# Optimization experiments

Hardware: AMD Instinct MI355X
Metric: run time of the kernel (lower is better)

Reference implementation:

```python
import jax, jax.numpy as jnp
import numpy as np

B = 131072      # batch
IN = 1024       # input_dim
H = 384         # hidden[0]
L = 128         # latent_dim = hidden[1]
K = 32          # slots_k
R = 2           # top_r
TAU = 0.7


def setup_inputs() -> dict:
    key = jax.random.key(0)
    ks = jax.random.split(key, 8)
    s = 0.02
    f32 = jnp.float32
    return {
        "x":  jax.random.normal(ks[0], (B, IN), f32),
        "w1": jax.random.normal(ks[1], (IN, H), f32) * s,
        "b1": jnp.zeros((H,), f32),
        "w2": jax.random.normal(ks[2], (H, L), f32) * s,
        "b2": jnp.zeros((L,), f32),
        "mk": jax.random.normal(ks[3], (K, L), f32) * s,  # memory_keys
        "mv": jax.random.normal(ks[4], (K, L), f32) * s,  # memory_values
        "w3": jax.random.normal(ks[5], (2 * L, H), f32) * s,
        "b3": jnp.zeros((H,), f32),
        "w4": jax.random.normal(ks[6], (H, 1), f32) * s,
        "b4": jnp.zeros((1,), f32),
    }


def reference(x, w1, b1, w2, b2, mk, mv, w3, b3, w4, b4):
    # block_a: Linear -> GELU -> (Dropout=id in eval) -> Linear -> GELU
    z = jax.nn.gelu(x @ w1 + b1, approximate=False)
    z = jax.nn.gelu(z @ w2 + b2, approximate=False)          # [B, L]

    # top-r slot attention over memory bank
    logits = (z @ mk.T) / TAU                                 # [B, K]
    _, idx = jax.lax.top_k(logits, R)                         # [B, R]
    keep = jax.nn.one_hot(idx, K, dtype=logits.dtype).sum(-2) > 0  # [B, K] bool
    masked = jnp.where(keep, logits, -jnp.inf)
    attn = jax.nn.softmax(masked, axis=-1)                    # [B, K]
    mem = attn @ mv                                           # [B, L]

    fused = jnp.concatenate([z, mem], axis=-1)                # [B, 2L]

    # default head: Linear -> GELU -> Linear(.,1)
    h = jax.nn.gelu(fused @ w3 + b3, approximate=False)
    logit = (h @ w4 + b4)[..., 0]                             # [B]
    return jax.nn.sigmoid(logit)
```

## Files before the change

kernel.cpp:

```cpp
#include <hip/hip_runtime.h>

#define BATCH   131072
#define INDIM   1024
#define BM      64
#define BDIM    512
#define NBLK    (BATCH / BM)

#define WT_OFF   0
#define XT0_OFF  49152
#define XT1_OFF  57344
#define Z1_OFF   0
#define W2T0_OFF 50176
#define W2T1_OFF 58368
#define FZ_OFF   0
#define RP_OFF   33792
#define W3T_OFF  42240
#define CB_OFF   66816
#define B1S_OFF  (CB_OFF)
#define B2S_OFF  (CB_OFF + 1536)
#define B3S_OFF  (CB_OFF + 2048)
#define W4S_OFF  (CB_OFF + 3584)
#define MKS_OFF  (CB_OFF + 5120)
#define SMEM_BYTES (CB_OFF + 13824)

typedef unsigned short u16;
typedef u16    u16x8  __attribute__((ext_vector_type(8)));
typedef u16    u16x4  __attribute__((ext_vector_type(4)));
typedef __bf16 bf16x8 __attribute__((ext_vector_type(8)));
typedef __bf16 bf16x4 __attribute__((ext_vector_type(4)));
typedef float  f32x4  __attribute__((ext_vector_type(4)));

__device__ __forceinline__ u16 f2bf(float f) {
  unsigned u = __float_as_uint(f);
  u += 0x7FFFu + ((u >> 16) & 1u);
  return (u16)(u >> 16);
}

__device__ __forceinline__ float gelu_fast(float v) {
  float t = v * v;
  float u = v * fmaf(t, 0.0356774081f, 0.7978845608f);
  float e = __builtin_amdgcn_exp2f(u * -2.885390082f);
  return v * __builtin_amdgcn_rcpf(1.0f + e);
}

__device__ __forceinline__ f32x4 mfma16(u16x8 a, u16x8 b, f32x4 c) {
  return __builtin_amdgcn_mfma_f32_16x16x32_bf16(
      __builtin_bit_cast(bf16x8, a), __builtin_bit_cast(bf16x8, b), c, 0, 0, 0);
}

__device__ __forceinline__ u16x8 cvt8(float4 a, float4 b) {
  bf16x8 r;
  r[0]=(__bf16)a.x; r[1]=(__bf16)a.y; r[2]=(__bf16)a.z; r[3]=(__bf16)a.w;
  r[4]=(__bf16)b.x; r[5]=(__bf16)b.y; r[6]=(__bf16)b.z; r[7]=(__bf16)b.w;
  return __builtin_bit_cast(u16x8, r);
}
__device__ __forceinline__ u16x4 cvt4(float4 a) {
  bf16x4 r;
  r[0]=(__bf16)a.x; r[1]=(__bf16)a.y; r[2]=(__bf16)a.z; r[3]=(__bf16)a.w;
  return __builtin_bit_cast(u16x4, r);
}

typedef __attribute__((address_space(3))) unsigned int       lds_u32;
typedef __attribute__((address_space(1))) const unsigned int glb_u32;
__device__ __forceinline__ void gload16(const void* g, void* l) {
  __builtin_amdgcn_global_load_lds((glb_u32*)g, (lds_u32*)l, 16, 0, 0);
}

#define FENCE_SCHED __builtin_amdgcn_sched_barrier(0)
#define WAIT_LGKM0 do { asm volatile("s_waitcnt lgkmcnt(0)" ::: "memory"); FENCE_SCHED; } while (0)
#define WAIT_VMN(N) do { asm volatile("s_waitcnt vmcnt(" #N ")" ::: "memory"); FENCE_SCHED; } while (0)
#define BARRIER_LGKM do { \
  asm volatile("s_waitcnt lgkmcnt(0)" ::: "memory"); \
  __builtin_amdgcn_s_barrier(); FENCE_SCHED; } while (0)

__global__ void prep_kernel(const float* __restrict__ w1, const float* __restrict__ w2,
                            const float* __restrict__ w3, u16* __restrict__ w1s,
                            u16* __restrict__ w2s, u16* __restrict__ w3s) {
  int i = blockIdx.x * 256 + threadIdx.x;
  if (i < 393216) {
    int t = i / 24576, p = i % 24576;
    int r = p >> 6, q = p & 63, cp = q >> 3, o = q & 7;
    int k = t * 64 + ((cp ^ (r & 7)) << 3) + o;
    w1s[i] = f2bf(w1[k * 384 + r]);
  } else if (i < 442368) {
    int j = i - 393216;
    int t = j / 4096, p = j % 4096;
    int r = p >> 5, q = p & 31, cp = q >> 3, o = q & 7;
    int k = t * 32 + ((cp ^ ((r >> 1) & 3)) << 3) + o;
    w2s[j] = f2bf(w2[k * 128 + r]);
  } else if (i < 540672) {
    int j = i - 442368;
    int t = j / 12288, p = j % 12288;
    int r = p >> 5, q = p & 31, cp = q >> 3, o = q & 7;
    int k = t * 32 + ((cp ^ ((r >> 1) & 3)) << 3) + o;
    w3s[j] = f2bf(w3[k * 384 + r]);
  }
}

__global__ __launch_bounds__(BDIM, 4) void fused_kernel(
    const float* __restrict__ x,  const u16* __restrict__ w1s,
    const float* __restrict__ b1, const u16* __restrict__ w2s,
    const float* __restrict__ b2, const float* __restrict__ mkw,
    const float* __restrict__ mvw, const u16* __restrict__ w3s,
    const float* __restrict__ b3, const float* __restrict__ w4,
    const float* __restrict__ b4, float* __restrict__ out) {
  extern __shared__ char smem[];
  u16*   z1  = (u16*)(smem + Z1_OFF);
  u16*   fz  = (u16*)(smem + FZ_OFF);
  u16*   w3t = (u16*)(smem + W3T_OFF);
  float* b1s = (float*)(smem + B1S_OFF);
  float* b2s = (float*)(smem + B2S_OFF);
  float* b3s = (float*)(smem + B3S_OFF);
  float* w4s = (float*)(smem + W4S_OFF);
  u16*   mks = (u16*)(smem + MKS_OFF);
  float* rowpart = (float*)(smem + RP_OFF);

  const int tid  = threadIdx.x;
  const int lane = tid & 63;
  const int wid  = tid >> 6;
  const int l15  = lane & 15;
  const int g    = lane >> 4;
  const int swz8 = l15 & 7;
  const int swz4 = (l15 >> 1) & 3;
  const int row0 = blockIdx.x * BM;
  const int wrow = wid * 48;
  const int wstrip = wid * 3072;

  {
    const u16* ws = w1s + wstrip + lane * 8;
    u16* wd = (u16*)(smem + WT_OFF) + wstrip;
    #pragma unroll
    for (int i = 0; i < 6; ++i) gload16(ws + i * 512, wd + i * 512);
  }
  FENCE_SCHED;
  const int xrow = tid >> 3, xoct = tid & 7;
  const float* xp = x + (long)(row0 + xrow) * INDIM + xoct * 8;
  const int xdst = xrow * 64 + ((xoct ^ (xrow & 7)) << 3);
  float4 xa = *(const float4*)xp, xb = *(const float4*)(xp + 4);

  if (tid < 384) b1s[tid] = b1[tid];
  if (tid < 128) b2s[tid] = b2[tid];
  if (tid < 384) b3s[tid] = b3[tid];
  if (tid < 384) w4s[tid] = w4[tid];
  {
    int r = tid >> 4, cc = (tid & 15) * 8;
    const float4* p = (const float4*)(mkw + r * 128 + cc);
    *(u16x8*)(mks + r * 136 + cc) = cvt8(p[0], p[1]);
  }
  *(u16x8*)((u16*)(smem + XT0_OFF) + xdst) = cvt8(xa, xb);
  { const float* p = xp + 64; xa = *(const float4*)p; xb = *(const float4*)(p + 4); }
  BARRIER_LGKM;

  f32x4 acc[4][3];
  #pragma unroll
  for (int m = 0; m < 4; ++m)
    #pragma unroll
    for (int n = 0; n < 3; ++n) acc[m][n] = (f32x4){0.f, 0.f, 0.f, 0.f};

  const u16* wtb = (const u16*)(smem + WT_OFF);
  for (int kt = 0; kt < 16; ++kt) {
    if (kt < 15) { WAIT_VMN(2); } else { WAIT_VMN(0); }
    const u16* xtb = (const u16*)(smem + ((kt & 1) ? XT1_OFF : XT0_OFF));
    u16x8 af[4], bfr[3];
    const int c0 = (g ^ swz8) * 8;
    #pragma unroll
    for (int m = 0; m < 4; ++m) af[m] = *(const u16x8*)(xtb + (m * 16 + l15) * 64 + c0);
    #pragma unroll
    for (int n = 0; n < 3; ++n) bfr[n] = *(const u16x8*)(wtb + (wrow + n * 16 + l15) * 64 + c0);
    #pragma unroll
    for (int m = 0; m < 4; ++m)
      #pragma unroll
      for (int n = 0; n < 3; ++n) acc[m][n] = mfma16(bfr[n], af[m], acc[m][n]);
    const int c1 = ((g + 4) ^ swz8) * 8;
    #pragma unroll
    for (int m = 0; m < 4; ++m) af[m] = *(const u16x8*)(xtb + (m * 16 + l15) * 64 + c1);
    #pragma unroll
    for (int n = 0; n < 3; ++n) bfr[n] = *(const u16x8*)(wtb + (wrow + n * 16 + l15) * 64 + c1);
    WAIT_LGKM0;
    if (kt < 15) {
      const u16* ws = w1s + (kt + 1) * 24576 + wstrip + lane * 8;
      u16* wd = (u16*)(smem + WT_OFF) + wstrip;
      #pragma unroll
      for (int i = 0; i < 6; ++i) gload16(ws + i * 512, wd + i * 512);
      FENCE_SCHED;
      u16* xn = (u16*)(smem + ((kt & 1) ? XT0_OFF : XT1_OFF));
      *(u16x8*)(xn + xdst) = cvt8(xa, xb);
      if (kt < 14) {
        const float* p = xp + (kt + 2) * 64;
        xa = *(const float4*)p; xb = *(const float4*)(p + 4);
      }
      BARRIER_LGKM;
    }
    #pragma unroll
    for (int m = 0; m < 4; ++m)
      #pragma unroll
      for (int n = 0; n < 3; ++n) acc[m][n] = mfma16(bfr[n], af[m], acc[m][n]);
  }
  BARRIER_LGKM;

  {
    const u16* s2 = w2s + wid * 512 + lane * 8;
    gload16(s2, (u16*)(smem + W2T0_OFF) + wid * 512);
    const u16* s2b = w2s + 4096 + wid * 512 + lane * 8;
    gload16(s2b, (u16*)(smem + W2T1_OFF) + wid * 512);
  }
  #pragma unroll
  for (int m = 0; m < 4; ++m) {
    #pragma unroll
    for (int n = 0; n < 3; ++n) {
      int col = wrow + n * 16 + g * 4;
      float4 bv = *(const float4*)(b1s + col);
      f32x4 a = acc[m][n];
      float4 gv = {gelu_fast(a[0] + bv.x), gelu_fast(a[1] + bv.y),
                   gelu_fast(a[2] + bv.z), gelu_fast(a[3] + bv.w)};
      *(u16x4*)(z1 + (m * 16 + l15) * 392 + col) = cvt4(gv);
    }
  }
  BARRIER_LGKM;

  f32x4 acc2[4];
  #pragma unroll
  for (int m = 0; m < 4; ++m) acc2[m] = (f32x4){0.f, 0.f, 0.f, 0.f};
  for (int kt = 0; kt < 12; ++kt) {
    if (kt < 10) { WAIT_VMN(1); } else { WAIT_VMN(0); }
    const u16* wb = (const u16*)(smem + ((kt & 1) ? W2T1_OFF : W2T0_OFF));
    u16x8 a2f[4];
    #pragma unroll
    for (int m = 0; m < 4; ++m)
      a2f[m] = *(const u16x8*)(z1 + (m * 16 + l15) * 392 + kt * 32 + g * 8);
    u16x8 b2f = *(const u16x8*)(wb + (wid * 16 + l15) * 32 + (g ^ swz4) * 8);
    WAIT_LGKM0;
    if (kt < 10) {
      const u16* s2 = w2s + (kt + 2) * 4096 + wid * 512 + lane * 8;
      gload16(s2, (u16*)(smem + ((kt & 1) ? W2T1_OFF : W2T0_OFF)) + wid * 512);
    }
    #pragma unroll
    for (int m = 0; m < 4; ++m) acc2[m] = mfma16(b2f, a2f[m], acc2[m]);
  }
  BARRIER_LGKM;

  {
    const u16* s3 = w3s + wid * 1536 + lane * 8;
    u16* d3 = w3t + wid * 1536;
    gload16(s3, d3); gload16(s3 + 512, d3 + 512); gload16(s3 + 1024, d3 + 1024);
  }
  #pragma unroll
  for (int m = 0; m < 4; ++m) {
    int col = wid * 16 + g * 4;
    float4 bv = *(const float4*)(b2s + col);
    f32x4 a = acc2[m];
    float4 gv = {gelu_fast(a[0] + bv.x), gelu_fast(a[1] + bv.y),
                 gelu_fast(a[2] + bv.z), gelu_fast(a[3] + bv.w)};
    *(u16x4*)(fz + (m * 16 + l15) * 264 + col) = cvt4(gv);
  }
  BARRIER_LGKM;

  if (wid < 4) {
    const int wr = wid * 16 + l15;
    f32x4 accl[2] = {(f32x4){0,0,0,0}, (f32x4){0,0,0,0}};
    #pragma unroll
    for (int ks = 0; ks < 4; ++ks) {
      u16x8 afz = *(const u16x8*)(fz + wr * 264 + ks * 32 + g * 8);
      u16x8 k0  = *(const u16x8*)(mks + l15 * 136 + ks * 32 + g * 8);
      u16x8 k1  = *(const u16x8*)(mks + (16 + l15) * 136 + ks * 32 + g * 8);
      accl[0] = mfma16(k0, afz, accl[0]);
      accl[1] = mfma16(k1, afz, accl[1]);
    }
    float m1 = -3.4e38f, m2 = -3.4e38f; int i1 = -1, i2 = -1;
    #pragma unroll
    for (int n = 0; n < 2; ++n)
      #pragma unroll
      for (int j = 0; j < 4; ++j) {
        float v = accl[n][j]; int idx = n * 16 + g * 4 + j;
        if (v > m1) { m2 = m1; i2 = i1; m1 = v; i1 = idx; }
        else if (v > m2) { m2 = v; i2 = idx; }
      }
    #pragma unroll
    for (int d = 16; d <= 32; d <<= 1) {
      float om1 = __shfl_xor(m1, d); int oi1 = __shfl_xor(i1, d);
      float om2 = __shfl_xor(m2, d); int oi2 = __shfl_xor(i2, d);
      bool take = (om1 > m1) || (om1 == m1 && oi1 < i1);
      if (take) {
        float nm2; int ni2;
        if (m1 > om2 || (m1 == om2 && i1 < oi2)) { nm2 = m1; ni2 = i1; }
        else { nm2 = om2; ni2 = oi2; }
        m1 = om1; i1 = oi1; m2 = nm2; i2 = ni2;
      } else {
        if (om1 > m2 || (om1 == m2 && oi1 < i2)) { m2 = om1; i2 = oi1; }
      }
    }
    float a1 = __builtin_amdgcn_rcpf(
        1.0f + __builtin_amdgcn_exp2f((m2 - m1) * (1.44269504f / 0.7f)));
    float a2 = 1.0f - a1;
    const float* v1 = mvw + i1 * 128 + g * 32;
    const float* v2 = mvw + i2 * 128 + g * 32;
    #pragma unroll
    for (int c = 0; c < 4; ++c) {
      float4 A0 = *(const float4*)(v1 + c * 8), A1 = *(const float4*)(v1 + c * 8 + 4);
      float4 B0 = *(const float4*)(v2 + c * 8), B1 = *(const float4*)(v2 + c * 8 + 4);
      float4 r0 = {a1*A0.x + a2*B0.x, a1*A0.y + a2*B0.y, a1*A0.z + a2*B0.z, a1*A0.w + a2*B0.w};
      float4 r1 = {a1*A1.x + a2*B1.x, a1*A1.y + a2*B1.y, a1*A1.z + a2*B1.z, a1*A1.w + a2*B1.w};
      *(u16x8*)(fz + wr * 264 + 128 + g * 32 + c * 8) = cvt8(r0, r1);
    }
  }
  BARRIER_LGKM;

  f32x4 acc3[4][3];
  #pragma unroll
  for (int m = 0; m < 4; ++m)
    #pragma unroll
    for (int n = 0; n < 3; ++n) acc3[m][n] = (f32x4){0.f, 0.f, 0.f, 0.f};
  for (int kt = 0; kt < 8; ++kt) {
    WAIT_VMN(0);
    u16x8 a3f[4], b3f[3];
    #pragma unroll
    for (int m = 0; m < 4; ++m)
      a3f[m] = *(const u16x8*)(fz + (m * 16 + l15) * 264 + kt * 32 + g * 8);
    #pragma unroll
    for (int n = 0; n < 3; ++n)
      b3f[n] = *(const u16x8*)(w3t + (wrow + n * 16 + l15) * 32 + (g ^ swz4) * 8);
    WAIT_LGKM0;
    if (kt < 7) {
      const u16* s3 = w3s + (kt + 1) * 12288 + wid * 1536 + lane * 8;
      u16* d3 = w3t + wid * 1536;
      gload16(s3, d3); gload16(s3 + 512, d3 + 512); gload16(s3 + 1024, d3 + 1024);
    }
    #pragma unroll
    for (int m = 0; m < 4; ++m)
      #pragma unroll
      for (int n = 0; n < 3; ++n) acc3[m][n] = mfma16(b3f[n], a3f[m], acc3[m][n]);
  }

  #pragma unroll
  for (int m = 0; m < 4; ++m) {
    float s = 0.f;
    #pragma unroll
    for (int n = 0; n < 3; ++n) {
      int col = wrow + n * 16 + g * 4;
      float4 bv = *(const float4*)(b3s + col);
      float4 wv = *(const float4*)(w4s + col);
      f32x4 a = acc3[m][n];
      s += gelu_fast(a[0] + bv.x) * wv.x + gelu_fast(a[1] + bv.y) * wv.y +
           gelu_fast(a[2] + bv.z) * wv.z + gelu_fast(a[3] + bv.w) * wv.w;
    }
    s += __shfl_xor(s, 16);
    s += __shfl_xor(s, 32);
    if (lane < 16) rowpart[(m * 16 + l15) * 8 + wid] = s;
  }
  BARRIER_LGKM;
  if (tid < BM) {
    const float4* rp = (const float4*)(rowpart + tid * 8);
    float4 p0 = rp[0], p1 = rp[1];
    float lg = b4[0] + p0.x + p0.y + p0.z + p0.w + p1.x + p1.y + p1.z + p1.w;
    out[row0 + tid] = __builtin_amdgcn_rcpf(1.0f + __builtin_amdgcn_exp2f(-lg * 1.44269504f));
  }
}

extern "C" void kernel_launch(void* const* d_in, const int* in_sizes, int n_in,
                              void* d_out, int out_size, void* d_ws, size_t ws_size,
                              hipStream_t stream) {
  const float* x  = (const float*)d_in[0];
  const float* w1 = (const float*)d_in[1];
  const float* b1 = (const float*)d_in[2];
  const float* w2 = (const float*)d_in[3];
  const float* b2 = (const float*)d_in[4];
  const float* mk = (const float*)d_in[5];
  const float* mv = (const float*)d_in[6];
  const float* w3 = (const float*)d_in[7];
  const float* b3 = (const float*)d_in[8];
  const float* w4 = (const float*)d_in[9];
  const float* b4 = (const float*)d_in[10];

  u16* w1s = (u16*)d_ws;
  u16* w2s = w1s + 393216;
  u16* w3s = w1s + 442368;

  prep_kernel<<<2112, 256, 0, stream>>>(w1, w2, w3, w1s, w2s, w3s);

  (void)hipFuncSetAttribute(reinterpret_cast<const void*>(fused_kernel),
                            hipFuncAttributeMaxDynamicSharedMemorySize, SMEM_BYTES);
  fused_kernel<<<NBLK, BDIM, SMEM_BYTES, stream>>>(x, w1s, b1, w2s, b2, mk, mv, w3s,
                                                   b3, w4, b4, (float*)d_out);
}
```

Before: 232.0 us.

## Double layer-1 K tile, double-buffer W3 and relax scheduling fences

Layer 1 now stages 128-wide K slices of x and W1 instead of 64, with a new 16-chunk swizzle applied in both the prep kernel and the LDS reads. This halves the number of K iterations and barriers. The W3 weight tile is double-buffered so its global-to-LDS loads overlap the layer-3 MFMAs. The sched_barrier fences after waitcnts are removed so the compiler can interleave work more freely. The cost is a much larger LDS footprint (about 145KB) and launch bounds lowered to 2, which cuts the number of resident blocks per CU and may reduce latency hiding.

```diff
diff --git a/kernel.cpp b/kernel.cpp
--- a/kernel.cpp
+++ b/kernel.cpp
@@ -7,15 +7,16 @@
 #define NBLK    (BATCH / BM)
 
 #define WT_OFF   0
-#define XT0_OFF  49152
-#define XT1_OFF  57344
+#define XT0_OFF  98304
+#define XT1_OFF  114688
 #define Z1_OFF   0
 #define W2T0_OFF 50176
 #define W2T1_OFF 58368
 #define FZ_OFF   0
 #define RP_OFF   33792
-#define W3T_OFF  42240
-#define CB_OFF   66816
+#define W3T0_OFF 42240
+#define W3T1_OFF 66816
+#define CB_OFF   131072
 #define B1S_OFF  (CB_OFF)
 #define B2S_OFF  (CB_OFF + 1536)
 #define B3S_OFF  (CB_OFF + 2048)
@@ -67,8 +68,8 @@
 }
 
 #define FENCE_SCHED __builtin_amdgcn_sched_barrier(0)
-#define WAIT_LGKM0 do { asm volatile("s_waitcnt lgkmcnt(0)" ::: "memory"); FENCE_SCHED; } while (0)
-#define WAIT_VMN(N) do { asm volatile("s_waitcnt vmcnt(" #N ")" ::: "memory"); FENCE_SCHED; } while (0)
+#define SOFT_LGKM0 asm volatile("s_waitcnt lgkmcnt(0)" ::: "memory")
+#define SOFT_VMN(N) asm volatile("s_waitcnt vmcnt(" #N ")" ::: "memory")
 #define BARRIER_LGKM do { \
   asm volatile("s_waitcnt lgkmcnt(0)" ::: "memory"); \
   __builtin_amdgcn_s_barrier(); FENCE_SCHED; } while (0)
@@ -78,9 +79,10 @@
                             u16* __restrict__ w2s, u16* __restrict__ w3s) {
   int i = blockIdx.x * 256 + threadIdx.x;
   if (i < 393216) {
-    int t = i / 24576, p = i % 24576;
-    int r = p >> 6, q = p & 63, cp = q >> 3, o = q & 7;
-    int k = t * 64 + ((cp ^ (r & 7)) << 3) + o;
+    int t = i / 49152, p = i % 49152;
+    int r = p >> 7, q = p & 127, cp = q >> 3, o = q & 7;
+    int cs = (cp & 8) | ((cp ^ (r & 7)) & 7);
+    int k = t * 128 + cs * 8 + o;
     w1s[i] = f2bf(w1[k * 384 + r]);
   } else if (i < 442368) {
     int j = i - 393216;
@@ -97,7 +99,7 @@
   }
 }
 
-__global__ __launch_bounds__(BDIM, 4) void fused_kernel(
+__global__ __launch_bounds__(BDIM, 2) void fused_kernel(
     const float* __restrict__ x,  const u16* __restrict__ w1s,
     const float* __restrict__ b1, const u16* __restrict__ w2s,
     const float* __restrict__ b2, const float* __restrict__ mkw,
@@ -107,7 +109,6 @@
   extern __shared__ char smem[];
   u16*   z1  = (u16*)(smem + Z1_OFF);
   u16*   fz  = (u16*)(smem + FZ_OFF);
-  u16*   w3t = (u16*)(smem + W3T_OFF);
   float* b1s = (float*)(smem + B1S_OFF);
   float* b2s = (float*)(smem + B2S_OFF);
   float* b3s = (float*)(smem + B3S_OFF);
@@ -120,23 +121,25 @@
   const int wid  = tid >> 6;
   const int l15  = lane & 15;
   const int g    = lane >> 4;
-  const int swz8 = l15 & 7;
   const int swz4 = (l15 >> 1) & 3;
   const int row0 = blockIdx.x * BM;
   const int wrow = wid * 48;
-  const int wstrip = wid * 3072;
+  const int wstrip = wid * 6144;
 
   {
     const u16* ws = w1s + wstrip + lane * 8;
     u16* wd = (u16*)(smem + WT_OFF) + wstrip;
     #pragma unroll
-    for (int i = 0; i < 6; ++i) gload16(ws + i * 512, wd + i * 512);
+    for (int i = 0; i < 12; ++i) gload16(ws + i * 512, wd + i * 512);
   }
   FENCE_SCHED;
-  const int xrow = tid >> 3, xoct = tid & 7;
-  const float* xp = x + (long)(row0 + xrow) * INDIM + xoct * 8;
-  const int xdst = xrow * 64 + ((xoct ^ (xrow & 7)) << 3);
-  float4 xa = *(const float4*)xp, xb = *(const float4*)(xp + 4);
+  const int xrow = tid >> 3, xq = tid & 7;
+  const float* xp = x + (long)(row0 + xrow) * INDIM + xq * 16;
+  const int c0 = 2 * xq, c1 = 2 * xq + 1;
+  const int s0 = ((c0 & 8) | ((c0 ^ (xrow & 7)) & 7)) * 8;
+  const int s1 = ((c1 & 8) | ((c1 ^ (xrow & 7)) & 7)) * 8;
+  float4 xa0 = *(const float4*)xp,        xa1 = *(const float4*)(xp + 4);
+  float4 xb0 = *(const float4*)(xp + 8),  xb1 = *(const float4*)(xp + 12);
 
   if (tid < 384) b1s[tid] = b1[tid];
   if (tid < 128) b2s[tid] = b2[tid];
@@ -144,11 +147,19 @@
   if (tid < 384) w4s[tid] = w4[tid];
   {
     int r = tid >> 4, cc = (tid & 15) * 8;
-    const float4* p = (const float4*)(mkw + r * 128 + cc);
-    *(u16x8*)(mks + r * 136 + cc) = cvt8(p[0], p[1]);
-  }
-  *(u16x8*)((u16*)(smem + XT0_OFF) + xdst) = cvt8(xa, xb);
-  { const float* p = xp + 64; xa = *(const float4*)p; xb = *(const float4*)(p + 4); }
+    const float4* pm = (const float4*)(mkw + r * 128 + cc);
+    *(u16x8*)(mks + r * 136 + cc) = cvt8(pm[0], pm[1]);
+  }
+  {
+    u16* xb = (u16*)(smem + XT0_OFF) + xrow * 128;
+    *(u16x8*)(xb + s0) = cvt8(xa0, xa1);
+    *(u16x8*)(xb + s1) = cvt8(xb0, xb1);
+  }
+  {
+    const float* p = xp + 128;
+    xa0 = *(const float4*)p;       xa1 = *(const float4*)(p + 4);
+    xb0 = *(const float4*)(p + 8); xb1 = *(const float4*)(p + 12);
+  }
   BARRIER_LGKM;
 
   f32x4 acc[4][3];
@@ -158,45 +169,44 @@
     for (int n = 0; n < 3; ++n) acc[m][n] = (f32x4){0.f, 0.f, 0.f, 0.f};
 
   const u16* wtb = (const u16*)(smem + WT_OFF);
-  for (int kt = 0; kt < 16; ++kt) {
-    if (kt < 15) { WAIT_VMN(2); } else { WAIT_VMN(0); }
+  for (int kt = 0; kt < 8; ++kt) {
+    if (kt < 7) { SOFT_VMN(4); } else { SOFT_VMN(0); }
     const u16* xtb = (const u16*)(smem + ((kt & 1) ? XT1_OFF : XT0_OFF));
-    u16x8 af[4], bfr[3];
-    const int c0 = (g ^ swz8) * 8;
-    #pragma unroll
-    for (int m = 0; m < 4; ++m) af[m] = *(const u16x8*)(xtb + (m * 16 + l15) * 64 + c0);
-    #pragma unroll
-    for (int n = 0; n < 3; ++n) bfr[n] = *(const u16x8*)(wtb + (wrow + n * 16 + l15) * 64 + c0);
-    #pragma unroll
-    for (int m = 0; m < 4; ++m)
-      #pragma unroll
-      for (int n = 0; n < 3; ++n) acc[m][n] = mfma16(bfr[n], af[m], acc[m][n]);
-    const int c1 = ((g + 4) ^ swz8) * 8;
-    #pragma unroll
-    for (int m = 0; m < 4; ++m) af[m] = *(const u16x8*)(xtb + (m * 16 + l15) * 64 + c1);
-    #pragma unroll
-    for (int n = 0; n < 3; ++n) bfr[n] = *(const u16x8*)(wtb + (wrow + n * 16 + l15) * 64 + c1);
-    WAIT_LGKM0;
-    if (kt < 15) {
-      const u16* ws = w1s + (kt + 1) * 24576 + wstrip + lane * 8;
-      u16* wd = (u16*)(smem + WT_OFF) + wstrip;
-      #pragma unroll
-      for (int i = 0; i < 6; ++i) gload16(ws + i * 512, wd + i * 512);
-      FENCE_SCHED;
-      u16* xn = (u16*)(smem + ((kt & 1) ? XT0_OFF : XT1_OFF));
-      *(u16x8*)(xn + xdst) = cvt8(xa, xb);
-      if (kt < 14) {
-        const float* p = xp + (kt + 2) * 64;
-        xa = *(const float4*)p; xb = *(const float4*)(p + 4);
-      }
-      BARRIER_LGKM;
-    }
-    #pragma unroll
-    for (int m = 0; m < 4; ++m)
-      #pragma unroll
-      for (int n = 0; n < 3; ++n) acc[m][n] = mfma16(bfr[n], af[m], acc[m][n]);
-  }
-  BARRIER_LGKM;
+    #pragma unroll
+    for (int s = 0; s < 4; ++s) {
+      const int c = s * 4 + g;
+      const int cs = ((c & 8) | ((c ^ (l15 & 7)) & 7)) * 8;
+      u16x8 af[4], bfr[3];
+      #pragma unroll
+      for (int m = 0; m < 4; ++m) af[m] = *(const u16x8*)(xtb + (m * 16 + l15) * 128 + cs);
+      #pragma unroll
+      for (int n = 0; n < 3; ++n) bfr[n] = *(const u16x8*)(wtb + (wrow + n * 16 + l15) * 128 + cs);
+      #pragma unroll
+      for (int m = 0; m < 4; ++m)
+        #pragma unroll
+        for (int n = 0; n < 3; ++n) acc[m][n] = mfma16(bfr[n], af[m], acc[m][n]);
+    }
+    SOFT_LGKM0;
+    if (kt < 7) {
+      {
+        const u16* ws = w1s + (kt + 1) * 49152 + wstrip + lane * 8;
+        u16* wd = (u16*)(smem + WT_OFF) + wstrip;
+        #pragma unroll
+        for (int i = 0; i < 12; ++i) gload16(ws + i * 512, wd + i * 512);
+      }
+      {
+        u16* xb = (u16*)(smem + ((kt & 1) ? XT0_OFF : XT1_OFF)) + xrow * 128;
+        *(u16x8*)(xb + s0) = cvt8(xa0, xa1);
+        *(u16x8*)(xb + s1) = cvt8(xb0, xb1);
+      }
+      if (kt < 6) {
+        const float* p = xp + (kt + 2) * 128;
+        xa0 = *(const float4*)p;       xa1 = *(const float4*)(p + 4);
+        xb0 = *(const float4*)(p + 8); xb1 = *(const float4*)(p + 12);
+      }
+    }
+    BARRIER_LGKM;
+  }
 
   {
     const u16* s2 = w2s + wid * 512 + lane * 8;
@@ -222,14 +232,14 @@
   #pragma unroll
   for (int m = 0; m < 4; ++m) acc2[m] = (f32x4){0.f, 0.f, 0.f, 0.f};
   for (int kt = 0; kt < 12; ++kt) {
-    if (kt < 10) { WAIT_VMN(1); } else { WAIT_VMN(0); }
+    if (kt < 11) { SOFT_VMN(1); } else { SOFT_VMN(0); }
     const u16* wb = (const u16*)(smem + ((kt & 1) ? W2T1_OFF : W2T0_OFF));
     u16x8 a2f[4];
     #pragma unroll
     for (int m = 0; m < 4; ++m)
       a2f[m] = *(const u16x8*)(z1 + (m * 16 + l15) * 392 + kt * 32 + g * 8);
     u16x8 b2f = *(const u16x8*)(wb + (wid * 16 + l15) * 32 + (g ^ swz4) * 8);
-    WAIT_LGKM0;
+    SOFT_LGKM0;
     if (kt < 10) {
       const u16* s2 = w2s + (kt + 2) * 4096 + wid * 512 + lane * 8;
       gload16(s2, (u16*)(smem + ((kt & 1) ? W2T1_OFF : W2T0_OFF)) + wid * 512);
@@ -241,8 +251,11 @@
 
   {
     const u16* s3 = w3s + wid * 1536 + lane * 8;
-    u16* d3 = w3t + wid * 1536;
+    u16* d3 = (u16*)(smem + W3T0_OFF) + wid * 1536;
     gload16(s3, d3); gload16(s3 + 512, d3 + 512); gload16(s3 + 1024, d3 + 1024);
+    const u16* s3b = w3s + 12288 + wid * 1536 + lane * 8;
+    u16* d3b = (u16*)(smem + W3T1_OFF) + wid * 1536;
+    gload16(s3b, d3b); gload16(s3b + 512, d3b + 512); gload16(s3b + 1024, d3b + 1024);
   }
   #pragma unroll
   for (int m = 0; m < 4; ++m) {
@@ -311,18 +324,19 @@
     #pragma unroll
     for (int n = 0; n < 3; ++n) acc3[m][n] = (f32x4){0.f, 0.f, 0.f, 0.f};
   for (int kt = 0; kt < 8; ++kt) {
-    WAIT_VMN(0);
+    if (kt < 7) { SOFT_VMN(3); } else { SOFT_VMN(0); }
+    const u16* wb = (const u16*)(smem + ((kt & 1) ? W3T1_OFF : W3T0_OFF));
     u16x8 a3f[4], b3f[3];
     #pragma unroll
     for (int m = 0; m < 4; ++m)
       a3f[m] = *(const u16x8*)(fz + (m * 16 + l15) * 264 + kt * 32 + g * 8);
     #pragma unroll
     for (int n = 0; n < 3; ++n)
-      b3f[n] = *(const u16x8*)(w3t + (wrow + n * 16 + l15) * 32 + (g ^ swz4) * 8);
-    WAIT_LGKM0;
-    if (kt < 7) {
-      const u16* s3 = w3s + (kt + 1) * 12288 + wid * 1536 + lane * 8;
-      u16* d3 = w3t + wid * 1536;
+      b3f[n] = *(const u16x8*)(wb + (wrow + n * 16 + l15) * 32 + (g ^ swz4) * 8);
+    SOFT_LGKM0;
+    if (kt < 6) {
+      const u16* s3 = w3s + (kt + 2) * 12288 + wid * 1536 + lane * 8;
+      u16* d3 = (u16*)(smem + ((kt & 1) ? W3T1_OFF : W3T0_OFF)) + wid * 1536;
       gload16(s3, d3); gload16(s3 + 512, d3 + 512); gload16(s3 + 1024, d3 + 1024);
     }
     #pragma unroll
```

Measured after the change: 279.7 us. 1.21x slower.
